# Kernel optimization log

Measured on AMD Instinct MI355X. Metric: run time of the kernel, lower is better.

The kernel has to match this reference:

```python
import jax, jax.numpy as jnp
import numpy as np

B, N, K, F, H = 4, 1024, 100, 42, 64


def setup_inputs() -> dict:
    key = jax.random.key(0)
    ks = jax.random.split(key, 10)
    return {
        "image": jax.random.normal(ks[0], (B, N, F), jnp.float32),
        "dfeat": jax.random.normal(ks[1], (B, N, K, F, 3), jnp.float32) * 0.1,
        "neighbor": jax.random.randint(ks[2], (B, N, K), 0, N + 1, jnp.int32),
        "Egroup_weight": jax.random.uniform(ks[3], (B, N, N), jnp.float32),
        "divider": jnp.ones((B, N), jnp.float32),
        # fitting-net params (single atom type), cfg [F, H, H, 1], tanh
        "W1": jax.random.normal(ks[4], (F, H), jnp.float32) * 0.1,
        "b1": jnp.zeros((H,), jnp.float32),
        "W2": jax.random.normal(ks[5], (H, H), jnp.float32) * 0.1,
        "b2": jnp.zeros((H,), jnp.float32),
        "W3": jax.random.normal(ks[6], (H, 1), jnp.float32) * 0.1,
        "b3": jnp.zeros((1,), jnp.float32),
    }


def reference(image, dfeat, neighbor, Egroup_weight, divider, W1, b1, W2, b2, W3, b3):
    b, n, f = image.shape
    k = neighbor.shape[-1]

    def energy(x):  # per-atom energy: [..., F] -> [...]
        h = jnp.tanh(x @ W1 + b1)
        h = jnp.tanh(h @ W2 + b2)
        return (h @ W3 + b3)[..., 0]

    Ei = energy(image)                                   # [B, N]
    # dEi/dFeat: each Ei depends only on its own feature row, so grad of sum
    # gives the per-atom Jacobian rows (the autograd=True f_FC path).
    dE = jax.grad(lambda x: energy(x).sum())(image)      # [B, N, F]
    Etot = jnp.sum(Ei, axis=1)                           # [B]

    # Fortran 1-based neighbor indices; row 0 of the padded table is zeros
    # (neighbor==0 means "no neighbor").
    dE_pad = jnp.concatenate([jnp.zeros((b, 1, f), dE.dtype), dE], axis=1)  # [B, N+1, F]
    flat = dE_pad.reshape(b * (n + 1), f)
    offs = jnp.repeat(jnp.arange(b, dtype=jnp.int32) * (n + 1), n * k)
    idx = neighbor.reshape(-1).astype(jnp.int32) + offs
    dEi_nb = flat[idx].reshape(b, n, k, f)               # gather   [B, N, K, F]
    # Force[b,i,:] = sum_j dE[neighbor(i,j)] . dfeat[b,i,j]  (reduce over K, F)
    Force = jnp.einsum('bnkf,bnkfd->bnd', dEi_nb, dfeat)  # [B, N, 3]
    return Etot, Ei, Force
```

## Files before the change

### kernel.cpp

```cpp
#include <hip/hip_runtime.h>

#define B 4
#define N 1024
#define K 100
#define F 42
#define H 64

#define PAIRS (K * F)
#define MF4   (PAIRS * 3 / 4)
#define QP    (PAIRS / 4)

#define APW 4
#define NWV 4
#define APB (APW * NWV)
#define PW  68
#define PX  44

typedef float f32x4 __attribute__((ext_vector_type(4)));

__global__ __launch_bounds__(256) void mlp_kernel(
    const float* __restrict__ image,
    const float* __restrict__ W1, const float* __restrict__ b1,
    const float* __restrict__ W2, const float* __restrict__ b2,
    const float* __restrict__ W3, const float* __restrict__ b3,
    float* __restrict__ Ei, float* __restrict__ dE)
{
    __shared__ __align__(16) float W1s[F][PW];
    __shared__ __align__(16) float W2s[H][PW];
    __shared__ __align__(16) float xsh[APB][PX];
    __shared__ __align__(16) float h1sh[NWV][APW][H];
    __shared__ __align__(16) float g2sh[NWV][APW][H];
    __shared__ __align__(16) float g1sh[NWV][APW][H];

    const int tid  = threadIdx.x;
    const int lane = tid & 63;
    const int wv   = tid >> 6;
    const int a0   = blockIdx.x * APB;
    const int aw   = a0 + wv * APW;

    for (int idx = tid; idx < F * H; idx += 256)
        W1s[idx >> 6][idx & 63] = W1[idx];
    for (int idx = tid; idx < H * H; idx += 256)
        W2s[idx >> 6][idx & 63] = W2[idx];
    for (int idx = tid; idx < APB * F; idx += 256) {
        const int a = idx / F, f = idx - a * F;
        xsh[a][f] = image[(size_t)a0 * F + idx];
    }
    __syncthreads();

    float acc[APW];
    {
        const float bb = b1[lane];
        #pragma unroll
        for (int a = 0; a < APW; ++a) acc[a] = bb;
    }
    #pragma unroll
    for (int fc = 0; fc < 10; ++fc) {
        float wv4[4];
        #pragma unroll
        for (int t = 0; t < 4; ++t) wv4[t] = W1s[4 * fc + t][lane];
        #pragma unroll
        for (int a = 0; a < APW; ++a) {
            const f32x4 xv = *(const f32x4*)&xsh[wv * APW + a][4 * fc];
            #pragma unroll
            for (int t = 0; t < 4; ++t) acc[a] = fmaf(xv[t], wv4[t], acc[a]);
        }
    }
    #pragma unroll
    for (int f = 40; f < F; ++f) {
        const float w = W1s[f][lane];
        #pragma unroll
        for (int a = 0; a < APW; ++a) acc[a] = fmaf(xsh[wv * APW + a][f], w, acc[a]);
    }
    float h1l[APW];
    #pragma unroll
    for (int a = 0; a < APW; ++a) {
        h1l[a] = tanhf(acc[a]);
        h1sh[wv][a][lane] = h1l[a];
    }
    __builtin_amdgcn_wave_barrier();

    {
        const float bb = b2[lane];
        #pragma unroll
        for (int a = 0; a < APW; ++a) acc[a] = bb;
    }
    #pragma unroll
    for (int jc = 0; jc < H / 4; ++jc) {
        float wv4[4];
        #pragma unroll
        for (int t = 0; t < 4; ++t) wv4[t] = W2s[4 * jc + t][lane];
        #pragma unroll
        for (int a = 0; a < APW; ++a) {
            const f32x4 hv = *(const f32x4*)&h1sh[wv][a][4 * jc];
            #pragma unroll
            for (int t = 0; t < 4; ++t) acc[a] = fmaf(hv[t], wv4[t], acc[a]);
        }
    }
    const float w3 = W3[lane];
    const float bias3 = b3[0];
    #pragma unroll
    for (int a = 0; a < APW; ++a) {
        const float h2 = tanhf(acc[a]);
        g2sh[wv][a][lane] = w3 * (1.0f - h2 * h2);
        float t = h2 * w3;
        #pragma unroll
        for (int off = 32; off > 0; off >>= 1) t += __shfl_down(t, off);
        if (lane == 0) Ei[aw + a] = t + bias3;
    }
    __builtin_amdgcn_wave_barrier();

    float s[APW] = {0.f, 0.f, 0.f, 0.f};
    #pragma unroll
    for (int ic = 0; ic < H / 4; ++ic) {
        const f32x4 wr = *(const f32x4*)&W2s[lane][4 * ic];
        #pragma unroll
        for (int a = 0; a < APW; ++a) {
            const f32x4 gv = *(const f32x4*)&g2sh[wv][a][4 * ic];
            #pragma unroll
            for (int t = 0; t < 4; ++t) s[a] = fmaf(wr[t], gv[t], s[a]);
        }
    }
    #pragma unroll
    for (int a = 0; a < APW; ++a)
        g1sh[wv][a][lane] = s[a] * (1.0f - h1l[a] * h1l[a]);
    __builtin_amdgcn_wave_barrier();

    if (lane < F) {
        float dx[APW] = {0.f, 0.f, 0.f, 0.f};
        #pragma unroll
        for (int ic = 0; ic < H / 4; ++ic) {
            const f32x4 wr = *(const f32x4*)&W1s[lane][4 * ic];
            #pragma unroll
            for (int a = 0; a < APW; ++a) {
                const f32x4 gv = *(const f32x4*)&g1sh[wv][a][4 * ic];
                #pragma unroll
                for (int t = 0; t < 4; ++t) dx[a] = fmaf(wr[t], gv[t], dx[a]);
            }
        }
        #pragma unroll
        for (int a = 0; a < APW; ++a)
            dE[(size_t)(aw + a) * F + lane] = dx[a];
    }
}

__global__ __launch_bounds__(256) void force_kernel(
    const float* __restrict__ dE, const float* __restrict__ dfeat,
    const int* __restrict__ neighbor, const float* __restrict__ Ei,
    float* __restrict__ force, float* __restrict__ Etot)
{
    __shared__ int   nsh[K];
    __shared__ float red[4][3];

    const int tid  = threadIdx.x;
    const int bid  = blockIdx.x;
    const int lane = tid & 63, wave = tid >> 6;

    if (bid >= B * N) {
        const int b = bid - B * N;
        float s = 0.0f;
        for (int i = tid; i < N; i += 256) s += Ei[b * N + i];
        #pragma unroll
        for (int off = 32; off > 0; off >>= 1) s += __shfl_down(s, off);
        if (lane == 0) red[wave][0] = s;
        __syncthreads();
        if (tid == 0)
            Etot[b] = (red[0][0] + red[1][0]) + (red[2][0] + red[3][0]);
        return;
    }

    const int bn = bid;
    const int b  = bn >> 10;

    if (tid < K) nsh[tid] = neighbor[bn * K + tid];
    __syncthreads();

    const f32x4* df4 = (const f32x4*)dfeat + (size_t)bn * MF4;
    const float* dEb = dE + (size_t)b * (N * F);

    float fx = 0.0f, fy = 0.0f, fz = 0.0f;

    #pragma unroll 1
    for (int it = 0; it < 4; ++it) {
        const int p4 = it * 256 + tid;
        const int p  = 4 * p4;
        const f32x4 d0 = df4[3 * p4 + 0];
        const f32x4 d1 = df4[3 * p4 + 1];
        const f32x4 d2 = df4[3 * p4 + 2];
        float e[4];
        #pragma unroll
        for (int q = 0; q < 4; ++q) {
            const int pp = p + q;
            const int k  = pp / F;
            const int f  = pp - k * F;
            const int nb = nsh[k];
            e[q] = (nb > 0) ? dEb[(nb - 1) * F + f] : 0.0f;
        }
        fx = fmaf(e[0], d0.x, fx); fy = fmaf(e[0], d0.y, fy); fz = fmaf(e[0], d0.z, fz);
        fx = fmaf(e[1], d0.w, fx); fy = fmaf(e[1], d1.x, fy); fz = fmaf(e[1], d1.y, fz);
        fx = fmaf(e[2], d1.z, fx); fy = fmaf(e[2], d1.w, fy); fz = fmaf(e[2], d2.x, fz);
        fx = fmaf(e[3], d2.y, fx); fy = fmaf(e[3], d2.z, fy); fz = fmaf(e[3], d2.w, fz);
    }
    if (tid < QP - 1024) {
        const int p4 = 1024 + tid;
        const int p  = 4 * p4;
        const f32x4 d0 = df4[3 * p4 + 0];
        const f32x4 d1 = df4[3 * p4 + 1];
        const f32x4 d2 = df4[3 * p4 + 2];
        float e[4];
        #pragma unroll
        for (int q = 0; q < 4; ++q) {
            const int pp = p + q;
            const int k  = pp / F;
            const int f  = pp - k * F;
            const int nb = nsh[k];
            e[q] = (nb > 0) ? dEb[(nb - 1) * F + f] : 0.0f;
        }
        fx = fmaf(e[0], d0.x, fx); fy = fmaf(e[0], d0.y, fy); fz = fmaf(e[0], d0.z, fz);
        fx = fmaf(e[1], d0.w, fx); fy = fmaf(e[1], d1.x, fy); fz = fmaf(e[1], d1.y, fz);
        fx = fmaf(e[2], d1.z, fx); fy = fmaf(e[2], d1.w, fy); fz = fmaf(e[2], d2.x, fz);
        fx = fmaf(e[3], d2.y, fx); fy = fmaf(e[3], d2.z, fy); fz = fmaf(e[3], d2.w, fz);
    }

    #pragma unroll
    for (int off = 32; off > 0; off >>= 1) {
        fx += __shfl_down(fx, off);
        fy += __shfl_down(fy, off);
        fz += __shfl_down(fz, off);
    }
    if (lane == 0) { red[wave][0] = fx; red[wave][1] = fy; red[wave][2] = fz; }
    __syncthreads();
    if (tid == 0) {
        force[bn * 3 + 0] = (red[0][0] + red[1][0]) + (red[2][0] + red[3][0]);
        force[bn * 3 + 1] = (red[0][1] + red[1][1]) + (red[2][1] + red[3][1]);
        force[bn * 3 + 2] = (red[0][2] + red[1][2]) + (red[2][2] + red[3][2]);
    }
}

extern "C" void kernel_launch(void* const* d_in, const int* in_sizes, int n_in,
                              void* d_out, int out_size, void* d_ws, size_t ws_size,
                              hipStream_t stream)
{
    const float* image    = (const float*)d_in[0];
    const float* dfeat    = (const float*)d_in[1];
    const int*   neighbor = (const int*)d_in[2];
    const float* W1 = (const float*)d_in[5];
    const float* b1 = (const float*)d_in[6];
    const float* W2 = (const float*)d_in[7];
    const float* b2 = (const float*)d_in[8];
    const float* W3 = (const float*)d_in[9];
    const float* b3 = (const float*)d_in[10];

    float* out   = (float*)d_out;
    float* Etot  = out;
    float* Ei    = out + B;
    float* Force = out + B + B * N;
    float* dE    = (float*)d_ws;

    mlp_kernel<<<(B * N) / APB, 256, 0, stream>>>(image, W1, b1, W2, b2, W3, b3, Ei, dE);
    force_kernel<<<B * N + B, 256, 0, stream>>>(dE, dfeat, neighbor, Ei, Force, Etot);
}
```

Measured before the change: 49.37 us.

## Keep MLP weights in registers and broadcast activations via readlane

The MLP kernel now caches each lane's W1/W2 column and row slices in registers and broadcasts per-atom activations with readlane, instead of staging x, h1, g2 and g1 through shared memory with wave barriers. W1 is zero-padded to 64 rows so the backward pass can loop over all H uniformly. This removes the LDS traffic and barriers in the forward and backward matvecs. In exchange it uses heavy register pressure (about 230 floats per lane), which is why launch bounds are pinned to one block, and it issues many serialized readlane operations.

New measurement: 51.77 us. 4.8% more time.

```diff
diff --git a/kernel.cpp b/kernel.cpp
--- a/kernel.cpp
+++ b/kernel.cpp
@@ -14,39 +14,52 @@
 #define NWV 4
 #define APB (APW * NWV)
 #define PW  68
-#define PX  44
 
 typedef float f32x4 __attribute__((ext_vector_type(4)));
 
-__global__ __launch_bounds__(256) void mlp_kernel(
+__device__ __forceinline__ float rl(float v, int l) {
+    return __int_as_float(__builtin_amdgcn_readlane(__float_as_int(v), l));
+}
+
+__global__ __launch_bounds__(256, 1) void mlp_kernel(
     const float* __restrict__ image,
     const float* __restrict__ W1, const float* __restrict__ b1,
     const float* __restrict__ W2, const float* __restrict__ b2,
     const float* __restrict__ W3, const float* __restrict__ b3,
     float* __restrict__ Ei, float* __restrict__ dE)
 {
-    __shared__ __align__(16) float W1s[F][PW];
+    __shared__ __align__(16) float W1s[H][PW];
     __shared__ __align__(16) float W2s[H][PW];
-    __shared__ __align__(16) float xsh[APB][PX];
-    __shared__ __align__(16) float h1sh[NWV][APW][H];
-    __shared__ __align__(16) float g2sh[NWV][APW][H];
-    __shared__ __align__(16) float g1sh[NWV][APW][H];
 
     const int tid  = threadIdx.x;
     const int lane = tid & 63;
     const int wv   = tid >> 6;
-    const int a0   = blockIdx.x * APB;
-    const int aw   = a0 + wv * APW;
-
-    for (int idx = tid; idx < F * H; idx += 256)
-        W1s[idx >> 6][idx & 63] = W1[idx];
-    for (int idx = tid; idx < H * H; idx += 256)
-        W2s[idx >> 6][idx & 63] = W2[idx];
-    for (int idx = tid; idx < APB * F; idx += 256) {
-        const int a = idx / F, f = idx - a * F;
-        xsh[a][f] = image[(size_t)a0 * F + idx];
+    const int aw   = blockIdx.x * APB + wv * APW;
+
+    for (int idx = tid; idx < H * H; idx += 256) {
+        const int r = idx >> 6, c = idx & 63;
+        W1s[r][c] = (r < F) ? W1[idx] : 0.0f;
+        W2s[r][c] = W2[idx];
     }
     __syncthreads();
+
+    float w1c[F];
+    #pragma unroll
+    for (int f = 0; f < F; ++f) w1c[f] = W1s[f][lane];
+    float w2c[H];
+    #pragma unroll
+    for (int j = 0; j < H; ++j) w2c[j] = W2s[j][lane];
+    f32x4 w2r[H / 4];
+    #pragma unroll
+    for (int i = 0; i < H / 4; ++i) w2r[i] = *(const f32x4*)&W2s[lane][4 * i];
+    f32x4 w1r[H / 4];
+    #pragma unroll
+    for (int i = 0; i < H / 4; ++i) w1r[i] = *(const f32x4*)&W1s[lane][4 * i];
+
+    float x[APW];
+    #pragma unroll
+    for (int a = 0; a < APW; ++a)
+        x[a] = (lane < F) ? image[(size_t)(aw + a) * F + lane] : 0.0f;
 
     float acc[APW];
     {
@@ -55,30 +68,14 @@
         for (int a = 0; a < APW; ++a) acc[a] = bb;
     }
     #pragma unroll
-    for (int fc = 0; fc < 10; ++fc) {
-        float wv4[4];
-        #pragma unroll
-        for (int t = 0; t < 4; ++t) wv4[t] = W1s[4 * fc + t][lane];
-        #pragma unroll
-        for (int a = 0; a < APW; ++a) {
-            const f32x4 xv = *(const f32x4*)&xsh[wv * APW + a][4 * fc];
-            #pragma unroll
-            for (int t = 0; t < 4; ++t) acc[a] = fmaf(xv[t], wv4[t], acc[a]);
-        }
-    }
-    #pragma unroll
-    for (int f = 40; f < F; ++f) {
-        const float w = W1s[f][lane];
-        #pragma unroll
-        for (int a = 0; a < APW; ++a) acc[a] = fmaf(xsh[wv * APW + a][f], w, acc[a]);
+    for (int f = 0; f < F; ++f) {
+        #pragma unroll
+        for (int a = 0; a < APW; ++a)
+            acc[a] = fmaf(rl(x[a], f), w1c[f], acc[a]);
     }
     float h1l[APW];
     #pragma unroll
-    for (int a = 0; a < APW; ++a) {
-        h1l[a] = tanhf(acc[a]);
-        h1sh[wv][a][lane] = h1l[a];
-    }
-    __builtin_amdgcn_wave_barrier();
+    for (int a = 0; a < APW; ++a) h1l[a] = tanhf(acc[a]);
 
     {
         const float bb = b2[lane];
@@ -86,58 +83,49 @@
         for (int a = 0; a < APW; ++a) acc[a] = bb;
     }
     #pragma unroll
-    for (int jc = 0; jc < H / 4; ++jc) {
-        float wv4[4];
-        #pragma unroll
-        for (int t = 0; t < 4; ++t) wv4[t] = W2s[4 * jc + t][lane];
-        #pragma unroll
-        for (int a = 0; a < APW; ++a) {
-            const f32x4 hv = *(const f32x4*)&h1sh[wv][a][4 * jc];
-            #pragma unroll
-            for (int t = 0; t < 4; ++t) acc[a] = fmaf(hv[t], wv4[t], acc[a]);
-        }
-    }
-    const float w3 = W3[lane];
+    for (int j = 0; j < H; ++j) {
+        #pragma unroll
+        for (int a = 0; a < APW; ++a)
+            acc[a] = fmaf(rl(h1l[a], j), w2c[j], acc[a]);
+    }
+
+    const float w3    = W3[lane];
     const float bias3 = b3[0];
+    float g2l[APW];
     #pragma unroll
     for (int a = 0; a < APW; ++a) {
         const float h2 = tanhf(acc[a]);
-        g2sh[wv][a][lane] = w3 * (1.0f - h2 * h2);
+        g2l[a] = w3 * (1.0f - h2 * h2);
         float t = h2 * w3;
         #pragma unroll
         for (int off = 32; off > 0; off >>= 1) t += __shfl_down(t, off);
         if (lane == 0) Ei[aw + a] = t + bias3;
     }
-    __builtin_amdgcn_wave_barrier();
-
-    float s[APW] = {0.f, 0.f, 0.f, 0.f};
-    #pragma unroll
-    for (int ic = 0; ic < H / 4; ++ic) {
-        const f32x4 wr = *(const f32x4*)&W2s[lane][4 * ic];
-        #pragma unroll
-        for (int a = 0; a < APW; ++a) {
-            const f32x4 gv = *(const f32x4*)&g2sh[wv][a][4 * ic];
+
+    float g1l[APW];
+    {
+        float s[APW] = {0.f, 0.f, 0.f, 0.f};
+        #pragma unroll
+        for (int i = 0; i < H; ++i) {
+            const float w = w2r[i >> 2][i & 3];
             #pragma unroll
-            for (int t = 0; t < 4; ++t) s[a] = fmaf(wr[t], gv[t], s[a]);
+            for (int a = 0; a < APW; ++a)
+                s[a] = fmaf(rl(g2l[a], i), w, s[a]);
         }
-    }
-    #pragma unroll
-    for (int a = 0; a < APW; ++a)
-        g1sh[wv][a][lane] = s[a] * (1.0f - h1l[a] * h1l[a]);
-    __builtin_amdgcn_wave_barrier();
-
+        #pragma unroll
+        for (int a = 0; a < APW; ++a)
+            g1l[a] = s[a] * (1.0f - h1l[a] * h1l[a]);
+    }
+
+    float dx[APW] = {0.f, 0.f, 0.f, 0.f};
+    #pragma unroll
+    for (int i = 0; i < H; ++i) {
+        const float w = w1r[i >> 2][i & 3];
+        #pragma unroll
+        for (int a = 0; a < APW; ++a)
+            dx[a] = fmaf(rl(g1l[a], i), w, dx[a]);
+    }
     if (lane < F) {
-        float dx[APW] = {0.f, 0.f, 0.f, 0.f};
-        #pragma unroll
-        for (int ic = 0; ic < H / 4; ++ic) {
-            const f32x4 wr = *(const f32x4*)&W1s[lane][4 * ic];
-            #pragma unroll
-            for (int a = 0; a < APW; ++a) {
-                const f32x4 gv = *(const f32x4*)&g1sh[wv][a][4 * ic];
-                #pragma unroll
-                for (int t = 0; t < 4; ++t) dx[a] = fmaf(wr[t], gv[t], dx[a]);
-            }
-        }
         #pragma unroll
         for (int a = 0; a < APW; ++a)
             dE[(size_t)(aw + a) * F + lane] = dx[a];
```
